# Optimization experiments

Hardware: AMD Instinct MI355X
Metric: run time of the kernel (lower is better)

The kernel has to match this reference:

```python
import jax, jax.numpy as jnp
import numpy as np


def setup_inputs() -> dict:
    key = jax.random.key(0)
    k1, k2 = jax.random.split(key)
    T, D, E = 8192, 4096, 64  # tokens, model_dim, num_experts
    x = jax.random.normal(k1, (T, D), dtype=jnp.float32)
    wg = jax.random.normal(k2, (E, D), dtype=jnp.float32) * (1.0 / np.sqrt(D))
    return {"x": x, "wg": wg}


def reference(x, wg):
    # gate logits: nn.Linear(model_dim, num_experts, bias=False) in fp32
    logits = jnp.einsum('td,ed->te', x.astype(jnp.float32), wg)  # [T, E]
    gates = jax.nn.softmax(logits, axis=1)                        # [T, E]
    # top1gating (eval mode: no noise): argmax over gates
    indices1_s = jnp.argmax(gates, axis=1)                        # [T] int
    # gates = (gates * one_hot(indices1_s)).sum(dim=1) == gather of the max gate
    gates1_s = jnp.take_along_axis(gates, indices1_s[:, None], axis=1)[:, 0]  # [T]
    return indices1_s, gates1_s
```

## Files before the change

### kernel.cpp

```cpp
#include <hip/hip_runtime.h>

typedef __attribute__((ext_vector_type(8))) short bf16x8;
typedef __attribute__((ext_vector_type(4))) float f32x4;

constexpr int TN = 8192;
constexpr int DN = 4096;
constexpr int EN = 64;

constexpr int BM = 32;
constexpr int NS = DN / 32;
constexpr int NT = 16;

__device__ __forceinline__ unsigned short f2bf(float f) {
    unsigned u = __builtin_bit_cast(unsigned, f);
    u += 0x7FFFu + ((u >> 16) & 1u);
    return (unsigned short)(u >> 16);
}
__device__ __forceinline__ float bf2f(unsigned short h) {
    unsigned u = ((unsigned)h) << 16;
    return __builtin_bit_cast(float, u);
}

__global__ __launch_bounds__(256)
void wg_frag_kernel(const float* __restrict__ wg, unsigned short* __restrict__ BF) {
    const int gid = blockIdx.x * 256 + threadIdx.x;
    const int l  = gid & 63;
    const int et = (gid >> 6) & 3;
    const int s  = (gid >> 8) & (NS - 1);
    const int p  = gid >> 15;
    const int e  = et * 16 + (l & 15);
    const int k  = s * 32 + (l >> 4) * 4;

    const float* src = wg + (size_t)e * DN + k;
    float4 v0 = *reinterpret_cast<const float4*>(src);
    float4 v1 = *reinterpret_cast<const float4*>(src + 16);
    float f[8] = {v0.x, v0.y, v0.z, v0.w, v1.x, v1.y, v1.z, v1.w};
    unsigned short o[8];
#pragma unroll
    for (int j = 0; j < 8; ++j) {
        unsigned short h = f2bf(f[j]);
        o[j] = p ? f2bf(f[j] - bf2f(h)) : h;
    }
    unsigned short* dst = BF + (((size_t)p * NS + s) * 4 + et) * 512 + (size_t)l * 8;
    *reinterpret_cast<ushort4*>(dst)     = make_ushort4(o[0], o[1], o[2], o[3]);
    *reinterpret_cast<ushort4*>(dst + 4) = make_ushort4(o[4], o[5], o[6], o[7]);
}

__global__ __launch_bounds__(512, 2)
void gate_fused_kernel(const float* __restrict__ x,
                       const unsigned short* __restrict__ BF,
                       float* __restrict__ out) {
    __shared__ float L[8][BM][68];

    const int tid  = threadIdx.x;
    const int lane = tid & 63;
    const int w    = tid >> 6;
    const int kq   = w & 3;
    const int kh   = w >> 2;
    const int r0   = blockIdx.x * BM;

    const int fr = lane & 15;
    const int g  = lane >> 4;

    const float* xa = x + (size_t)(r0 + fr) * DN + g * 4;

    f32x4 acc[2][4] = {};

    float4 XA[3][2][2];
    bf16x8 Bq[2][8];

    auto loadA = [&](int set, int t) {
        const int s = kh * 64 + t * 4 + kq;
        const float* p = xa + (size_t)s * 32;
#pragma unroll
        for (int rh = 0; rh < 2; ++rh) {
            const float* pr = p + (size_t)rh * 16 * DN;
            XA[set][rh][0] = *reinterpret_cast<const float4*>(pr);
            XA[set][rh][1] = *reinterpret_cast<const float4*>(pr + 16);
        }
    };
    auto loadB = [&](int set, int t) {
        const int s = kh * 64 + t * 4 + kq;
        const unsigned short* bp = BF + (size_t)s * 2048 + (size_t)lane * 8;
#pragma unroll
        for (int et = 0; et < 4; ++et)
            Bq[set][et] = *reinterpret_cast<const bf16x8*>(bp + et * 512);
#pragma unroll
        for (int et = 0; et < 4; ++et)
            Bq[set][4 + et] = *reinterpret_cast<const bf16x8*>(bp + (size_t)NS * 2048 + et * 512);
    };
    auto compute = [&](int aset, int bset) {
        bf16x8 ah[2], al[2];
#pragma unroll
        for (int rh = 0; rh < 2; ++rh) {
            float f[8] = {XA[aset][rh][0].x, XA[aset][rh][0].y,
                          XA[aset][rh][0].z, XA[aset][rh][0].w,
                          XA[aset][rh][1].x, XA[aset][rh][1].y,
                          XA[aset][rh][1].z, XA[aset][rh][1].w};
#pragma unroll
            for (int j = 0; j < 8; ++j) {
                unsigned short hh = f2bf(f[j]);
                ah[rh][j] = (short)hh;
                al[rh][j] = (short)f2bf(f[j] - bf2f(hh));
            }
        }
#pragma unroll
        for (int et = 0; et < 4; ++et)
#pragma unroll
            for (int rh = 0; rh < 2; ++rh) {
                acc[rh][et] = __builtin_amdgcn_mfma_f32_16x16x32_bf16(ah[rh], Bq[bset][et],     acc[rh][et], 0, 0, 0);
                acc[rh][et] = __builtin_amdgcn_mfma_f32_16x16x32_bf16(al[rh], Bq[bset][et],     acc[rh][et], 0, 0, 0);
                acc[rh][et] = __builtin_amdgcn_mfma_f32_16x16x32_bf16(ah[rh], Bq[bset][4 + et], acc[rh][et], 0, 0, 0);
                acc[rh][et] = __builtin_amdgcn_mfma_f32_16x16x32_bf16(al[rh], Bq[bset][4 + et], acc[rh][et], 0, 0, 0);
            }
    };

    loadB(0, 0);
    loadA(0, 0);
    loadB(1, 1);
    loadA(1, 1);
    loadA(2, 2);
#pragma unroll
    for (int t = 0; t < NT; ++t) {
        compute(t % 3, t & 1);
        if (t + 2 < NT) loadB(t & 1, t + 2);
        if (t + 3 < NT) loadA(t % 3, t + 3);
        asm volatile("" ::: "memory");
    }

#pragma unroll
    for (int rh = 0; rh < 2; ++rh)
#pragma unroll
        for (int et = 0; et < 4; ++et)
#pragma unroll
            for (int r = 0; r < 4; ++r)
                L[w][rh * 16 + g * 4 + r][et * 16 + fr] = acc[rh][et][r];
    __syncthreads();

    {
        const int row = tid >> 4;
        const int eg  = tid & 15;
        float v[4];
#pragma unroll
        for (int j = 0; j < 4; ++j) {
            float s = L[0][row][eg * 4 + j];
#pragma unroll
            for (int q = 1; q < 8; ++q) s += L[q][row][eg * 4 + j];
            v[j] = s;
        }
        float m = v[0];
        int idx = eg * 4;
#pragma unroll
        for (int j = 1; j < 4; ++j)
            if (v[j] > m) { m = v[j]; idx = eg * 4 + j; }
#pragma unroll
        for (int d = 1; d < 16; d <<= 1) {
            float om = __shfl_xor(m, d);
            int   oi = __shfl_xor(idx, d);
            if (om > m || (om == m && oi < idx)) { m = om; idx = oi; }
        }
        float s = 0.0f;
#pragma unroll
        for (int j = 0; j < 4; ++j) s += __expf(v[j] - m);
#pragma unroll
        for (int d = 1; d < 16; d <<= 1) s += __shfl_xor(s, d);
        if (eg == 0) {
            out[r0 + row]      = (float)idx;
            out[TN + r0 + row] = 1.0f / s;
        }
    }
}

extern "C" void kernel_launch(void* const* d_in, const int* in_sizes, int n_in,
                              void* d_out, int out_size, void* d_ws, size_t ws_size,
                              hipStream_t stream) {
    const float* x  = (const float*)d_in[0];
    const float* wg = (const float*)d_in[1];
    float* out = (float*)d_out;

    unsigned short* BF = (unsigned short*)d_ws;

    wg_frag_kernel<<<dim3(256), dim3(256), 0, stream>>>(wg, BF);
    gate_fused_kernel<<<dim3(TN / BM), dim3(512), 0, stream>>>(x, BF, out);
}
```

Baseline: 37.47 us.

## Split-K gate GEMM across blocks with LDS-staged weights and separate reduction kernel

Restructures the gate GEMM so each block handles 256 rows and one of 8 K-slices, staging that slice of the bf16 hi/lo weight fragments in LDS once rather than having every wave read them from global memory. Each wave now owns 32 rows over the block's K-slice and writes fp32 partial logits to a workspace. A third kernel then sums the 8 partials per row and does argmax and softmax. The aim is to cut repeated global weight traffic and increase x-row reuse per block, at the cost of an extra launch and extra partial-sum traffic through global memory.

After: 54.43 us. 1.45x slower.

```diff
diff --git a/kernel.cpp b/kernel.cpp
--- a/kernel.cpp
+++ b/kernel.cpp
@@ -7,9 +7,10 @@
 constexpr int DN = 4096;
 constexpr int EN = 64;
 
-constexpr int BM = 32;
-constexpr int NS = DN / 32;
-constexpr int NT = 16;
+constexpr int NS     = DN / 32;
+constexpr int KSPLIT = 8;
+constexpr int SLOTS  = NS / KSPLIT;
+constexpr int RB     = 256;
 
 __device__ __forceinline__ unsigned short f2bf(float f) {
     unsigned u = __builtin_bit_cast(unsigned, f);
@@ -46,32 +47,41 @@
     *reinterpret_cast<ushort4*>(dst + 4) = make_ushort4(o[4], o[5], o[6], o[7]);
 }
 
-__global__ __launch_bounds__(512, 2)
-void gate_fused_kernel(const float* __restrict__ x,
-                       const unsigned short* __restrict__ BF,
-                       float* __restrict__ out) {
-    __shared__ float L[8][BM][68];
+__global__ __launch_bounds__(512, 1)
+void gate_gemm_kernel(const float* __restrict__ x,
+                      const unsigned short* __restrict__ BF,
+                      float* __restrict__ part) {
+    __shared__ uint4 LB[SLOTS * 2 * 256];
 
     const int tid  = threadIdx.x;
     const int lane = tid & 63;
     const int w    = tid >> 6;
-    const int kq   = w & 3;
-    const int kh   = w >> 2;
-    const int r0   = blockIdx.x * BM;
+    const int rt   = blockIdx.x >> 3;
+    const int ks   = blockIdx.x & 7;
+    const int r0   = rt * RB;
 
     const int fr = lane & 15;
     const int g  = lane >> 4;
 
-    const float* xa = x + (size_t)(r0 + fr) * DN + g * 4;
+    {
+        const uint4* gsrc = reinterpret_cast<const uint4*>(BF);
+#pragma unroll
+        for (int i = 0; i < SLOTS * 2 * 256 / 512; ++i) {
+            int e = tid + i * 512;
+            int j = e & 255, p = (e >> 8) & 1, s = e >> 9;
+            LB[e] = gsrc[((size_t)p * NS + ks * SLOTS + s) * 256 + j];
+        }
+    }
+    __syncthreads();
+
+    const float* xa = x + (size_t)(r0 + w * 32 + fr) * DN + g * 4;
 
     f32x4 acc[2][4] = {};
-
     float4 XA[3][2][2];
-    bf16x8 Bq[2][8];
+    bf16x8 Bh[2][4], Bl[2][4];
 
     auto loadA = [&](int set, int t) {
-        const int s = kh * 64 + t * 4 + kq;
-        const float* p = xa + (size_t)s * 32;
+        const float* p = xa + (size_t)(ks * SLOTS + t) * 32;
 #pragma unroll
         for (int rh = 0; rh < 2; ++rh) {
             const float* pr = p + (size_t)rh * 16 * DN;
@@ -80,14 +90,12 @@
         }
     };
     auto loadB = [&](int set, int t) {
-        const int s = kh * 64 + t * 4 + kq;
-        const unsigned short* bp = BF + (size_t)s * 2048 + (size_t)lane * 8;
 #pragma unroll
         for (int et = 0; et < 4; ++et)
-            Bq[set][et] = *reinterpret_cast<const bf16x8*>(bp + et * 512);
+            Bh[set][et] = __builtin_bit_cast(bf16x8, LB[(t * 2 + 0) * 256 + et * 64 + lane]);
 #pragma unroll
         for (int et = 0; et < 4; ++et)
-            Bq[set][4 + et] = *reinterpret_cast<const bf16x8*>(bp + (size_t)NS * 2048 + et * 512);
+            Bl[set][et] = __builtin_bit_cast(bf16x8, LB[(t * 2 + 1) * 256 + et * 64 + lane]);
     };
     auto compute = [&](int aset, int bset) {
         bf16x8 ah[2], al[2];
@@ -108,67 +116,65 @@
         for (int et = 0; et < 4; ++et)
 #pragma unroll
             for (int rh = 0; rh < 2; ++rh) {
-                acc[rh][et] = __builtin_amdgcn_mfma_f32_16x16x32_bf16(ah[rh], Bq[bset][et],     acc[rh][et], 0, 0, 0);
-                acc[rh][et] = __builtin_amdgcn_mfma_f32_16x16x32_bf16(al[rh], Bq[bset][et],     acc[rh][et], 0, 0, 0);
-                acc[rh][et] = __builtin_amdgcn_mfma_f32_16x16x32_bf16(ah[rh], Bq[bset][4 + et], acc[rh][et], 0, 0, 0);
-                acc[rh][et] = __builtin_amdgcn_mfma_f32_16x16x32_bf16(al[rh], Bq[bset][4 + et], acc[rh][et], 0, 0, 0);
+                acc[rh][et] = __builtin_amdgcn_mfma_f32_16x16x32_bf16(ah[rh], Bh[bset][et], acc[rh][et], 0, 0, 0);
+                acc[rh][et] = __builtin_amdgcn_mfma_f32_16x16x32_bf16(al[rh], Bh[bset][et], acc[rh][et], 0, 0, 0);
+                acc[rh][et] = __builtin_amdgcn_mfma_f32_16x16x32_bf16(ah[rh], Bl[bset][et], acc[rh][et], 0, 0, 0);
+                acc[rh][et] = __builtin_amdgcn_mfma_f32_16x16x32_bf16(al[rh], Bl[bset][et], acc[rh][et], 0, 0, 0);
             }
     };
 
-    loadB(0, 0);
     loadA(0, 0);
-    loadB(1, 1);
     loadA(1, 1);
     loadA(2, 2);
+    loadB(0, 0);
 #pragma unroll
-    for (int t = 0; t < NT; ++t) {
+    for (int t = 0; t < SLOTS; ++t) {
+        if (t + 1 < SLOTS) loadB((t + 1) & 1, t + 1);
         compute(t % 3, t & 1);
-        if (t + 2 < NT) loadB(t & 1, t + 2);
-        if (t + 3 < NT) loadA(t % 3, t + 3);
+        if (t + 3 < SLOTS) loadA(t % 3, t + 3);
         asm volatile("" ::: "memory");
     }
 
+    float* dst = part + ((size_t)ks * TN + r0 + w * 32) * EN;
 #pragma unroll
     for (int rh = 0; rh < 2; ++rh)
 #pragma unroll
         for (int et = 0; et < 4; ++et)
 #pragma unroll
             for (int r = 0; r < 4; ++r)
-                L[w][rh * 16 + g * 4 + r][et * 16 + fr] = acc[rh][et][r];
-    __syncthreads();
+                dst[(size_t)(rh * 16 + g * 4 + r) * EN + et * 16 + fr] = acc[rh][et][r];
+}
 
-    {
-        const int row = tid >> 4;
-        const int eg  = tid & 15;
-        float v[4];
+__global__ __launch_bounds__(256)
+void top1_softmax_kernel(const float* __restrict__ part, float* __restrict__ out) {
+    const int row = blockIdx.x * blockDim.x + threadIdx.x;
+    if (row >= TN) return;
+
+    float v[EN];
 #pragma unroll
-        for (int j = 0; j < 4; ++j) {
-            float s = L[0][row][eg * 4 + j];
+    for (int i = 0; i < EN / 4; ++i) {
+        float4 s = *reinterpret_cast<const float4*>(&part[(size_t)row * EN + i * 4]);
 #pragma unroll
-            for (int q = 1; q < 8; ++q) s += L[q][row][eg * 4 + j];
-            v[j] = s;
+        for (int h = 1; h < KSPLIT; ++h) {
+            float4 t = *reinterpret_cast<const float4*>(
+                &part[((size_t)h * TN + row) * EN + i * 4]);
+            s.x += t.x; s.y += t.y; s.z += t.z; s.w += t.w;
         }
-        float m = v[0];
-        int idx = eg * 4;
+        v[i * 4 + 0] = s.x; v[i * 4 + 1] = s.y;
+        v[i * 4 + 2] = s.z; v[i * 4 + 3] = s.w;
+    }
+
+    float m = v[0];
+    int idx = 0;
 #pragma unroll
-        for (int j = 1; j < 4; ++j)
-            if (v[j] > m) { m = v[j]; idx = eg * 4 + j; }
+    for (int e = 1; e < EN; ++e)
+        if (v[e] > m) { m = v[e]; idx = e; }
+    float s = 0.0f;
 #pragma unroll
-        for (int d = 1; d < 16; d <<= 1) {
-            float om = __shfl_xor(m, d);
-            int   oi = __shfl_xor(idx, d);
-            if (om > m || (om == m && oi < idx)) { m = om; idx = oi; }
-        }
-        float s = 0.0f;
-#pragma unroll
-        for (int j = 0; j < 4; ++j) s += __expf(v[j] - m);
-#pragma unroll
-        for (int d = 1; d < 16; d <<= 1) s += __shfl_xor(s, d);
-        if (eg == 0) {
-            out[r0 + row]      = (float)idx;
-            out[TN + r0 + row] = 1.0f / s;
-        }
-    }
+    for (int e = 0; e < EN; ++e) s += __expf(v[e] - m);
+
+    out[row]      = (float)idx;
+    out[TN + row] = 1.0f / s;
 }
 
 extern "C" void kernel_launch(void* const* d_in, const int* in_sizes, int n_in,
@@ -178,8 +184,11 @@
     const float* wg = (const float*)d_in[1];
     float* out = (float*)d_out;
 
+    constexpr size_t BF_BYTES = (size_t)2 * NS * 4 * 512 * 2;
     unsigned short* BF = (unsigned short*)d_ws;
+    float* part = (float*)((char*)d_ws + BF_BYTES);
 
     wg_frag_kernel<<<dim3(256), dim3(256), 0, stream>>>(wg, BF);
-    gate_fused_kernel<<<dim3(TN / BM), dim3(512), 0, stream>>>(x, BF, out);
+    gate_gemm_kernel<<<dim3((TN / RB) * KSPLIT), dim3(512), 0, stream>>>(x, BF, part);
+    top1_softmax_kernel<<<dim3(TN / 256), dim3(256), 0, stream>>>(part, out);
 }
```
